# Kernel tuning notes

Measured on AMD Instinct MI355X. Metric: run time of the kernel, lower is better.

Reference implementation:

```python
import jax, jax.numpy as jnp
import numpy as np

EPS = 1e-20
K, STRIDE, PAD = 5, 2, 2
B, CIN, COUT, H, W = 4, 32, 32, 192, 192
HO = (H + 2 * PAD - K) // STRIDE + 1
WO = (W + 2 * PAD - K) // STRIDE + 1


def _patches(x, pad_value):
    # x: [B,C,H,W] -> [B,C,K*K,HO,WO]; same window layout as F.max_pool2d
    xp = jnp.pad(x, ((0, 0), (0, 0), (PAD, PAD), (PAD, PAD)), constant_values=pad_value)
    cols = [xp[:, :, dy:dy + STRIDE * HO:STRIDE, dx:dx + STRIDE * WO:STRIDE]
            for dy in range(K) for dx in range(K)]
    return jnp.stack(cols, axis=2)


def setup_inputs() -> dict:
    key = jax.random.key(0)
    ks = jax.random.split(key, 9)
    d = jax.random.uniform(ks[0], (B, CIN, H, W), jnp.float32, 0.05, 1.0)
    cd = jax.random.uniform(ks[1], (B, CIN, H, W), jnp.float32)
    s = jax.random.uniform(ks[2], (B, CIN, H, W), jnp.float32)
    cs = jax.random.uniform(ks[3], (B, CIN, H, W), jnp.float32)
    w_s_from_d = jax.random.normal(ks[4], (1, 1, 1, 1), jnp.float32) * 0.5
    w_prop = jax.random.normal(ks[5], (1, CIN, 1, 1), jnp.float32) * 0.5
    spatial_weight = jax.random.normal(ks[6], (CIN, 1, K, K), jnp.float32) * 0.5
    channel_weight = jax.random.normal(ks[7], (COUT, CIN, 1, 1), jnp.float32) * 0.5
    bias = jax.random.normal(ks[8], (1, COUT, 1, 1), jnp.float32) * 0.1
    return {"d": d, "cd": cd, "s": s, "cs": cs, "w_s_from_d": w_s_from_d,
            "w_prop": w_prop, "spatial_weight": spatial_weight,
            "channel_weight": channel_weight, "bias": bias}


def reference(d, cd, s, cs, w_s_from_d, w_prop, spatial_weight, channel_weight, bias):
    # EnforcePos reparameterization applied at forward time
    w_sfd = jax.nn.sigmoid(w_s_from_d)
    w_p = jax.nn.softplus(w_prop)
    sw = jax.nn.softplus(spatial_weight)   # [CIN,1,K,K] depthwise
    cw = jax.nn.softplus(channel_weight)   # [COUT,CIN,1,1]

    # max-pool argmax indices (torch pads with -inf), then gather d/cd at those indices
    j_max = jnp.argmax(_patches(d * cd, -jnp.inf), axis=2, keepdims=True)
    j_min = jnp.argmax(_patches(cd / (d + EPS), -jnp.inf), axis=2, keepdims=True)
    p_d = _patches(d, 0.0)
    p_cd = _patches(cd, 0.0)
    d_max = jnp.take_along_axis(p_d, j_max, axis=2)[:, :, 0]
    d_min = jnp.take_along_axis(p_d, j_min, axis=2)[:, :, 0]
    cd_max = jnp.take_along_axis(p_cd, j_max, axis=2)[:, :, 0]
    cd_min = jnp.take_along_axis(p_cd, j_min, axis=2)[:, :, 0]

    min_div_max = jnp.abs(d_min / (d_max + EPS))
    s_from_d = (1 - w_sfd) * min_div_max + w_sfd * min_div_max ** 2
    cs_from_d = cd_max * cd_min

    # stride > 1: no pre-propagation
    s_prop, cs_prop = s, cs

    dn = ('NCHW', 'OIHW', 'NCHW')
    def dwconv(x):  # depthwise 5x5, stride 2, pad 2
        return jax.lax.conv_general_dilated(
            x, sw, (STRIDE, STRIDE), [(PAD, PAD), (PAD, PAD)],
            feature_group_count=CIN, dimension_numbers=dn)

    nom = dwconv(cs_prop * s_prop)
    denom = dwconv(cs_prop)
    s_spatial = nom / (denom + EPS)
    cs_spatial = denom / (jnp.sum(sw) + EPS)

    cw2 = cw[:, :, 0, 0]  # [COUT,CIN], 1x1 conv == channel mixing
    nom = jnp.einsum('bihw,oi->bohw', cs_spatial * s_spatial, cw2)
    denom = jnp.einsum('bihw,oi->bohw', cs_spatial, cw2)
    s_out = nom / (denom + EPS)
    cs_out = denom / (jnp.sum(cw) + EPS)

    # stride > 1: merge pooled s_from_d afterwards
    s_out = (w_p * cs_out * s_out + cs_from_d * s_from_d) / (w_p * cs_out + cs_from_d + EPS)
    cs_out = (w_p * cs_out + cs_from_d) / (w_p + 1)

    s_out = s_out + bias
    s_out = jax.nn.sigmoid(s_out * 2 - 1) / 2 + 0.5
    return s_out, cs_out / (STRIDE * STRIDE)
```

## Files before the change

kernel.cpp:

```cpp
#include <hip/hip_runtime.h>

#define KK    5
#define PADV  2
#define NB    4
#define NC    32
#define NH    192
#define NW    192
#define NHO   96
#define NWO   96
#define NPX   (NHO * NWO)
#define NPLANE (NB * NC * NPX)
#define EPSF  1e-20f

__device__ __forceinline__ float softplusf(float x) {
    return fmaxf(x, 0.f) + log1pf(expf(-fabsf(x)));
}

#define TROWS 19
#define NJ    98
#define PLD4  100
#define K1T   768
#define ITEMS (TROWS * NJ)

__global__ __launch_bounds__(K1T, 6) void k1(
    const float* __restrict__ dg,
    const float* __restrict__ cdg,
    const float* __restrict__ sg,
    const float* __restrict__ csg,
    const float* __restrict__ wsfdg,
    const float* __restrict__ spwg,
    float4* __restrict__ ws4)
{
    __shared__ float4 st_e[TROWS][PLD4];
    __shared__ float4 st_o[TROWS][PLD4];
    __shared__ float sw_row[25];
    __shared__ float red[12];
    __shared__ float scal[2];

    const int t  = threadIdx.x;
    const int bx = blockIdx.x;
    const int c  = blockIdx.y;
    const int b  = blockIdx.z;

    const int gy0 = 16 * bx - 2;
    const size_t base = ((size_t)(b * NC) + c) * (NH * NW);

    float2 Ld[3], Lcd[3], Ls[3], Lcs[3];
    int   rr_[3], jj_[3];
    bool  okv[3], act[3];
#pragma unroll
    for (int k = 0; k < 3; k++) {
        const int it = t + k * K1T;
        act[k] = (it < ITEMS);
        const int r = act[k] ? (it / NJ) : 0;
        const int j = act[k] ? (it - r * NJ) : 0;
        rr_[k] = r; jj_[k] = j;
        const int gy = gy0 + r;
        const bool ok = act[k] && ((unsigned)gy < NH) && (j >= 1) && (j <= 96);
        okv[k] = ok;
        float2 z = make_float2(0.f, 0.f);
        Ld[k] = z; Lcd[k] = z; Ls[k] = z; Lcs[k] = z;
        if (ok) {
            const size_t idx = base + (size_t)gy * NW + (2 * j - 2);
            Ld[k]  = *(const float2*)(dg  + idx);
            Lcd[k] = *(const float2*)(cdg + idx);
            Ls[k]  = *(const float2*)(sg  + idx);
            Lcs[k] = *(const float2*)(csg + idx);
        }
    }

    float part = 0.f;
    for (int i = t; i < NC * 25; i += K1T) {
        float v = softplusf(spwg[i]);
        part += v;
        int cr = i - c * 25;
        if (cr >= 0 && cr < 25) sw_row[cr] = v;
    }
#pragma unroll
    for (int m = 32; m >= 1; m >>= 1) part += __shfl_xor(part, m, 64);
    if ((t & 63) == 0) red[t >> 6] = part;

#pragma unroll
    for (int k = 0; k < 3; k++) {
        if (act[k]) {
            float pme, pve, pmo, pvo;
            if (okv[k]) {
                pme = Ld[k].x * Lcd[k].x;
                pve = Lcd[k].x / (Ld[k].x + EPSF);
                pmo = Ld[k].y * Lcd[k].y;
                pvo = Lcd[k].y / (Ld[k].y + EPSF);
            } else {
                pme = -INFINITY; pve = -INFINITY; pmo = -INFINITY; pvo = -INFINITY;
            }
            const int r = rr_[k], j = jj_[k];
            st_e[r][j] = make_float4(pme, pve, Lcs[k].x, Lcs[k].x * Ls[k].x);
            st_o[r][j] = make_float4(pmo, pvo, Lcs[k].y, Lcs[k].y * Ls[k].y);
        }
    }
    __syncthreads();
    if (t == 0) {
        float acc = 0.f;
#pragma unroll
        for (int i = 0; i < 12; i++) acc += red[i];
        scal[0] = acc;
        scal[1] = 1.f / (1.f + expf(-wsfdg[0]));
    }
    __syncthreads();

    const int oyl = t / 96;
    const int ox  = t - oyl * 96;
    const int r0  = oyl * 2;

    float bm = -INFINITY, bv = -INFINITY;
    float pvm = 0.f, pmn = 0.f;
    float nom = 0.f, den = 0.f;

#pragma unroll
    for (int dy = 0; dy < 5; dy++) {
        const int r = r0 + dy;
        const float w0 = sw_row[dy * 5 + 0];
        const float w1 = sw_row[dy * 5 + 1];
        const float w2 = sw_row[dy * 5 + 2];
        const float w3 = sw_row[dy * 5 + 3];
        const float w4 = sw_row[dy * 5 + 4];

        const float4 E0 = st_e[r][ox];
        const float4 O0 = st_o[r][ox];
        const float4 E1 = st_e[r][ox + 1];
        const float4 O1 = st_o[r][ox + 1];
        const float4 E2 = st_e[r][ox + 2];

        if (E0.x > bm) { bm = E0.x; pvm = E0.y; }
        if (E0.y > bv) { bv = E0.y; pmn = E0.x; }
        if (O0.x > bm) { bm = O0.x; pvm = O0.y; }
        if (O0.y > bv) { bv = O0.y; pmn = O0.x; }
        if (E1.x > bm) { bm = E1.x; pvm = E1.y; }
        if (E1.y > bv) { bv = E1.y; pmn = E1.x; }
        if (O1.x > bm) { bm = O1.x; pvm = O1.y; }
        if (O1.y > bv) { bv = O1.y; pmn = O1.x; }
        if (E2.x > bm) { bm = E2.x; pvm = E2.y; }
        if (E2.y > bv) { bv = E2.y; pmn = E2.x; }

        nom += w0 * E0.w; den += w0 * E0.z;
        nom += w1 * O0.w; den += w1 * O0.z;
        nom += w2 * E1.w; den += w2 * E1.z;
        nom += w3 * O1.w; den += w3 * O1.z;
        nom += w4 * E2.w; den += w4 * E2.z;
    }

    const float t1 = pmn * pvm;
    const float t2 = bv * bm;
    const float mdm = fabsf(sqrtf(t1 / t2));
    const float cfd = sqrtf(t1 * t2);

    const float sumsw = scal[0];
    const float wsfd  = scal[1];
    const float sfd  = (1.f - wsfd) * mdm + wsfd * mdm * mdm;
    const float ssp  = nom / (den + EPSF);
    const float cssp = den / (sumsw + EPSF);

    const int opx = (8 * bx + oyl) * NWO + ox;
    const size_t oidx = ((size_t)(b * NC) + c) * NPX + opx;
    ws4[oidx] = make_float4(cssp * ssp, cssp, sfd, cfd);
}

#define K2PX 32

__global__ __launch_bounds__(256, 8) void k2(
    const float4* __restrict__ ws4,
    const float* __restrict__ wpropg,
    const float* __restrict__ chwg,
    const float* __restrict__ biasg,
    float* __restrict__ out)
{
    __shared__ float cw_s[NC * NC];
    __shared__ float wp_s[NC];
    __shared__ float bias_s[NC];
    __shared__ float A_s[NC][K2PX + 1];
    __shared__ float B_s[NC][K2PX + 1];
    __shared__ float S_s[NC][K2PX + 1];
    __shared__ float C_s[NC][K2PX + 1];
    __shared__ float red[4];
    __shared__ float scal[1];

    const int t    = threadIdx.x;
    const int b    = blockIdx.y;
    const int px0  = blockIdx.x * K2PX;
    const int p    = t & (K2PX - 1);
    const int slot = t >> 5;

    float part = 0.f;
    for (int i = t; i < NC * NC; i += 256) {
        float v = softplusf(chwg[i]); cw_s[i] = v; part += v;
    }
    if (t < NC) { wp_s[t] = softplusf(wpropg[t]); bias_s[t] = biasg[t]; }
#pragma unroll
    for (int m = 32; m >= 1; m >>= 1) part += __shfl_xor(part, m, 64);
    if ((t & 63) == 0) red[t >> 6] = part;

    const size_t bb = (size_t)b * NC * NPX;
#pragma unroll
    for (int idx = 0; idx < NC * K2PX; idx += 256) {
        const int i  = (idx + t) >> 5;
        const int pp = (idx + t) & (K2PX - 1);
        const float4 q = ws4[bb + (size_t)i * NPX + px0 + pp];
        A_s[i][pp] = q.x;
        B_s[i][pp] = q.y;
        S_s[i][pp] = q.z;
        C_s[i][pp] = q.w;
    }
    __syncthreads();
    if (t == 0) scal[0] = red[0] + red[1] + red[2] + red[3];
    __syncthreads();

    const float sumcw = scal[0];
    const int px = px0 + p;

    float nom2[4], den2[4];
#pragma unroll
    for (int k = 0; k < 4; k++) { nom2[k] = 0.f; den2[k] = 0.f; }

#pragma unroll
    for (int i = 0; i < NC; i++) {
        const float a  = A_s[i][p];
        const float b2 = B_s[i][p];
#pragma unroll
        for (int k = 0; k < 4; k++) {
            const float w = cw_s[(slot + 8 * k) * NC + i];
            nom2[k] += w * a;
            den2[k] += w * b2;
        }
    }

#pragma unroll
    for (int k = 0; k < 4; k++) {
        const int o = slot + 8 * k;
        const float sfd = S_s[o][p];
        const float cfd = C_s[o][p];

        const float smix  = nom2[k] / (den2[k] + EPSF);
        const float csmix = den2[k] / (sumcw + EPSF);
        const float wp    = wp_s[o];

        float sout = (wp * csmix * smix + cfd * sfd) / (wp * csmix + cfd + EPSF);
        const float csout = (wp * csmix + cfd) / (wp + 1.f);

        sout += bias_s[o];
        sout = 1.f / (1.f + expf(-(sout * 2.f - 1.f))) * 0.5f + 0.5f;

        const size_t oidx = bb + (size_t)o * NPX + px;
        out[oidx]                  = sout;
        out[(size_t)NPLANE + oidx] = csout * 0.25f;
    }
}

#define TW    8
#define TH    4
#define TPP   33

__global__ __launch_bounds__(256, 4) void fused_kernel(
    const float* __restrict__ dg,
    const float* __restrict__ cdg,
    const float* __restrict__ sg,
    const float* __restrict__ csg,
    const float* __restrict__ wsfdg,
    const float* __restrict__ wpropg,
    const float* __restrict__ spwg,
    const float* __restrict__ chwg,
    const float* __restrict__ biasg,
    float* __restrict__ out)
{
    __shared__ float sw_s[NC * 25];
    __shared__ float cw_s[NC * NC];
    __shared__ float wp_s[NC];
    __shared__ float bias_s[NC];
    __shared__ float A_s[NC][TPP];
    __shared__ float B_s[NC][TPP];
    __shared__ float S_s[NC][TPP];
    __shared__ float C_s[NC][TPP];
    __shared__ float red[8];
    __shared__ float scal[3];

    const int t = threadIdx.x;
    const int b = blockIdx.z;
    const int tile_x = blockIdx.x * TW;
    const int tile_y = blockIdx.y * TH;

    float p_sw = 0.f, p_cw = 0.f;
    for (int i = t; i < NC * 25; i += 256) { float v = softplusf(spwg[i]); sw_s[i] = v; p_sw += v; }
    for (int i = t; i < NC * NC; i += 256) { float v = softplusf(chwg[i]); cw_s[i] = v; p_cw += v; }
    if (t < NC) { wp_s[t] = softplusf(wpropg[t]); bias_s[t] = biasg[t]; }
#pragma unroll
    for (int m = 32; m >= 1; m >>= 1) {
        p_sw += __shfl_xor(p_sw, m, 64);
        p_cw += __shfl_xor(p_cw, m, 64);
    }
    if ((t & 63) == 0) { red[(t >> 6) * 2] = p_sw; red[(t >> 6) * 2 + 1] = p_cw; }
    __syncthreads();
    if (t == 0) {
        scal[0] = red[0] + red[2] + red[4] + red[6];
        scal[1] = red[1] + red[3] + red[5] + red[7];
        scal[2] = 1.f / (1.f + expf(-wsfdg[0]));
    }
    __syncthreads();

    const float sumsw = scal[0];
    const float sumcw = scal[1];
    const float wsfd  = scal[2];

    const int c  = t >> 3;
    const int tr = (t >> 2) & 1;
    const int q  = t & 3;
    const int oy0 = tile_y + tr * 2;
    const int ox0 = tile_x + q * 2;
    const int cb = ox0 * 2 - 2;
    const int rb = oy0 * 2 - 2;
    const size_t base = ((size_t)(b * NC) + c) * NH * NW;
    const float* __restrict__ dp  = dg  + base;
    const float* __restrict__ cdp = cdg + base;
    const float* __restrict__ sp  = sg  + base;
    const float* __restrict__ csp = csg + base;

    bool slotok[4];
#pragma unroll
    for (int k = 0; k < 4; k++) slotok[k] = (cb + 2 * k >= 0) && (cb + 2 * k + 1 < NW);
    bool ciok[7];
#pragma unroll
    for (int ci = 0; ci < 7; ci++) ciok[ci] = ((unsigned)(cb + ci) < NW);

    float bm[2][2], dM[2][2], cM[2][2];
    float bn[2][2], dN[2][2], cN[2][2];
    float nom[2][2], den[2][2];
#pragma unroll
    for (int r = 0; r < 2; r++)
#pragma unroll
        for (int q2 = 0; q2 < 2; q2++) {
            bm[r][q2] = -INFINITY; bn[r][q2] = -INFINITY;
            dM[r][q2] = 0.f; cM[r][q2] = 0.f; dN[r][q2] = 0.f; cN[r][q2] = 0.f;
            nom[r][q2] = 0.f; den[r][q2] = 0.f;
        }

#pragma unroll
    for (int rr = 0; rr < 7; rr++) {
        const int iy = rb + rr;
        if ((unsigned)iy < NH) {
            const int roff = iy * NW + cb;
            float dv[8], cdv[8], sv[8], csv[8];
#pragma unroll
            for (int k = 0; k < 4; k++) {
                float2 vD, vCD, vS, vCS;
                if (slotok[k]) {
                    vD  = *(const float2*)(dp  + roff + 2 * k);
                    vCD = *(const float2*)(cdp + roff + 2 * k);
                    vS  = *(const float2*)(sp  + roff + 2 * k);
                    vCS = *(const float2*)(csp + roff + 2 * k);
                } else {
                    vD = make_float2(0.f, 0.f); vCD = vD; vS = vD; vCS = vD;
                }
                dv[2*k] = vD.x;  dv[2*k+1] = vD.y;
                cdv[2*k] = vCD.x; cdv[2*k+1] = vCD.y;
                sv[2*k] = vS.x;  sv[2*k+1] = vS.y;
                csv[2*k] = vCS.x; csv[2*k+1] = vCS.y;
            }
            float pm[7], pv[7];
#pragma unroll
            for (int ci = 0; ci < 7; ci++) {
                pm[ci] = dv[ci] * cdv[ci];
                pv[ci] = cdv[ci] / (dv[ci] + EPSF);
            }
#pragma unroll
            for (int r = 0; r < 2; r++) {
                const int dy = rr - 2 * r;
                if (dy >= 0 && dy <= 4) {
#pragma unroll
                    for (int dx = 0; dx < 5; dx++) {
                        const float w = sw_s[c * 25 + dy * 5 + dx];
#pragma unroll
                        for (int q2 = 0; q2 < 2; q2++) {
                            const int ci = 2 * q2 + dx;
                            if (ciok[ci]) {
                                if (pm[ci] > bm[r][q2]) { bm[r][q2] = pm[ci]; dM[r][q2] = dv[ci]; cM[r][q2] = cdv[ci]; }
                                if (pv[ci] > bn[r][q2]) { bn[r][q2] = pv[ci]; dN[r][q2] = dv[ci]; cN[r][q2] = cdv[ci]; }
                                nom[r][q2] += w * (csv[ci] * sv[ci]);
                                den[r][q2] += w * csv[ci];
                            }
                        }
                    }
                }
            }
        }
    }

#pragma unroll
    for (int r = 0; r < 2; r++)
#pragma unroll
        for (int q2 = 0; q2 < 2; q2++) {
            const float mdm  = fabsf(dN[r][q2] / (dM[r][q2] + EPSF));
            const float sfd  = (1.f - wsfd) * mdm + wsfd * mdm * mdm;
            const float cfd  = cM[r][q2] * cN[r][q2];
            const float ssp  = nom[r][q2] / (den[r][q2] + EPSF);
            const float cssp = den[r][q2] / (sumsw + EPSF);
            const int p = (tr * 2 + r) * TW + (q * 2 + q2);
            A_s[c][p] = cssp * ssp;
            B_s[c][p] = cssp;
            S_s[c][p] = sfd;
            C_s[c][p] = cfd;
        }
    __syncthreads();

    const int p  = t & 31;
    const int o0 = t >> 5;
    const int py = p >> 3;
    const int pxx = p & 7;
    const int opx = (tile_y + py) * NWO + tile_x + pxx;

    float nom2[4], den2[4];
#pragma unroll
    for (int k = 0; k < 4; k++) { nom2[k] = 0.f; den2[k] = 0.f; }

#pragma unroll
    for (int i = 0; i < NC; i++) {
        const float a  = A_s[i][p];
        const float b2 = B_s[i][p];
#pragma unroll
        for (int k = 0; k < 4; k++) {
            const float w = cw_s[(o0 + 8 * k) * NC + i];
            nom2[k] += w * a;
            den2[k] += w * b2;
        }
    }

#pragma unroll
    for (int k = 0; k < 4; k++) {
        const int o = o0 + 8 * k;
        const float smix  = nom2[k] / (den2[k] + EPSF);
        const float csmix = den2[k] / (sumcw + EPSF);
        const float wp    = wp_s[o];
        const float sfd   = S_s[o][p];
        const float cfd   = C_s[o][p];

        float sout = (wp * csmix * smix + cfd * sfd) / (wp * csmix + cfd + EPSF);
        const float csout = (wp * csmix + cfd) / (wp + 1.f);

        sout += bias_s[o];
        sout = 1.f / (1.f + expf(-(sout * 2.f - 1.f))) * 0.5f + 0.5f;

        const int oidx = ((b * NC) + o) * NPX + opx;
        out[oidx]          = sout;
        out[NPLANE + oidx] = csout * 0.25f;
    }
}

extern "C" void kernel_launch(void* const* d_in, const int* in_sizes, int n_in,
                              void* d_out, int out_size, void* d_ws, size_t ws_size,
                              hipStream_t stream) {
    const float* d     = (const float*)d_in[0];
    const float* cd    = (const float*)d_in[1];
    const float* s     = (const float*)d_in[2];
    const float* cs    = (const float*)d_in[3];
    const float* wsfd  = (const float*)d_in[4];
    const float* wprop = (const float*)d_in[5];
    const float* spw   = (const float*)d_in[6];
    const float* chw   = (const float*)d_in[7];
    const float* bias  = (const float*)d_in[8];
    float* out = (float*)d_out;

    const size_t need = (size_t)4 * NPLANE * sizeof(float);
    if (ws_size >= need) {
        float4* ws4 = (float4*)d_ws;
        k1<<<dim3(NHO / 8, NC, NB), K1T, 0, stream>>>(d, cd, s, cs, wsfd, spw, ws4);
        k2<<<dim3(NPX / K2PX, NB), 256, 0, stream>>>(ws4, wprop, chw, bias, out);
    } else {
        fused_kernel<<<dim3(NWO / TW, NHO / TH, NB), 256, 0, stream>>>(
            d, cd, s, cs, wsfd, wprop, spw, chw, bias, out);
    }
}
```

Baseline: 41.45 us.

## Process three row strips per k1 block with register-prefetched next strip

Each k1 block now handles three consecutive 8-output-row strips instead of one, cutting the grid from 12 to 4 blocks along the row dimension. The global loads for the next strip are issued into registers while the current strip's pooling and depthwise conv run from shared memory, overlapping memory latency with compute. The per-block softplus weight setup and reduction is amortized over three strips. In exchange the grid has a third as many blocks (512), which may reduce occupancy and latency hiding across the GPU, and an extra barrier is added per strip.

```diff
diff --git a/kernel.cpp b/kernel.cpp
--- a/kernel.cpp
+++ b/kernel.cpp
@@ -20,6 +20,7 @@
 #define NJ    98
 #define PLD4  100
 #define K1T   768
+#define SPB   3
 #define ITEMS (TROWS * NJ)
 
 __global__ __launch_bounds__(K1T, 6) void k1(
@@ -38,16 +39,13 @@
     __shared__ float scal[2];
 
     const int t  = threadIdx.x;
-    const int bx = blockIdx.x;
+    const int sg0 = blockIdx.x * SPB;
     const int c  = blockIdx.y;
     const int b  = blockIdx.z;
-
-    const int gy0 = 16 * bx - 2;
     const size_t base = ((size_t)(b * NC) + c) * (NH * NW);
 
-    float2 Ld[3], Lcd[3], Ls[3], Lcs[3];
-    int   rr_[3], jj_[3];
-    bool  okv[3], act[3];
+    int  rr_[3], jj_[3];
+    bool act[3], jok[3];
 #pragma unroll
     for (int k = 0; k < 3; k++) {
         const int it = t + k * K1T;
@@ -55,17 +53,27 @@
         const int r = act[k] ? (it / NJ) : 0;
         const int j = act[k] ? (it - r * NJ) : 0;
         rr_[k] = r; jj_[k] = j;
-        const int gy = gy0 + r;
-        const bool ok = act[k] && ((unsigned)gy < NH) && (j >= 1) && (j <= 96);
-        okv[k] = ok;
-        float2 z = make_float2(0.f, 0.f);
-        Ld[k] = z; Lcd[k] = z; Ls[k] = z; Lcs[k] = z;
-        if (ok) {
-            const size_t idx = base + (size_t)gy * NW + (2 * j - 2);
-            Ld[k]  = *(const float2*)(dg  + idx);
-            Lcd[k] = *(const float2*)(cdg + idx);
-            Ls[k]  = *(const float2*)(sg  + idx);
-            Lcs[k] = *(const float2*)(csg + idx);
+        jok[k] = (j >= 1) && (j <= 96);
+    }
+
+    float2 Ld[3], Lcd[3], Ls[3], Lcs[3];
+    bool okv[3];
+    {
+        const int gy0 = 16 * sg0 - 2;
+#pragma unroll
+        for (int k = 0; k < 3; k++) {
+            const int gy = gy0 + rr_[k];
+            const bool ok = act[k] && ((unsigned)gy < NH) && jok[k];
+            okv[k] = ok;
+            float2 z = make_float2(0.f, 0.f);
+            Ld[k] = z; Lcd[k] = z; Ls[k] = z; Lcs[k] = z;
+            if (ok) {
+                const size_t idx = base + (size_t)gy * NW + (2 * jj_[k] - 2);
+                Ld[k]  = *(const float2*)(dg  + idx);
+                Lcd[k] = *(const float2*)(cdg + idx);
+                Ls[k]  = *(const float2*)(sg  + idx);
+                Lcs[k] = *(const float2*)(csg + idx);
+            }
         }
     }
 
@@ -79,24 +87,6 @@
 #pragma unroll
     for (int m = 32; m >= 1; m >>= 1) part += __shfl_xor(part, m, 64);
     if ((t & 63) == 0) red[t >> 6] = part;
-
-#pragma unroll
-    for (int k = 0; k < 3; k++) {
-        if (act[k]) {
-            float pme, pve, pmo, pvo;
-            if (okv[k]) {
-                pme = Ld[k].x * Lcd[k].x;
-                pve = Lcd[k].x / (Ld[k].x + EPSF);
-                pmo = Ld[k].y * Lcd[k].y;
-                pvo = Lcd[k].y / (Ld[k].y + EPSF);
-            } else {
-                pme = -INFINITY; pve = -INFINITY; pmo = -INFINITY; pvo = -INFINITY;
-            }
-            const int r = rr_[k], j = jj_[k];
-            st_e[r][j] = make_float4(pme, pve, Lcs[k].x, Lcs[k].x * Ls[k].x);
-            st_o[r][j] = make_float4(pmo, pvo, Lcs[k].y, Lcs[k].y * Ls[k].y);
-        }
-    }
     __syncthreads();
     if (t == 0) {
         float acc = 0.f;
@@ -106,62 +96,106 @@
         scal[1] = 1.f / (1.f + expf(-wsfdg[0]));
     }
     __syncthreads();
+    const float sumsw = scal[0];
+    const float wsfd  = scal[1];
 
     const int oyl = t / 96;
     const int ox  = t - oyl * 96;
     const int r0  = oyl * 2;
 
-    float bm = -INFINITY, bv = -INFINITY;
-    float pvm = 0.f, pmn = 0.f;
-    float nom = 0.f, den = 0.f;
-
-#pragma unroll
-    for (int dy = 0; dy < 5; dy++) {
-        const int r = r0 + dy;
-        const float w0 = sw_row[dy * 5 + 0];
-        const float w1 = sw_row[dy * 5 + 1];
-        const float w2 = sw_row[dy * 5 + 2];
-        const float w3 = sw_row[dy * 5 + 3];
-        const float w4 = sw_row[dy * 5 + 4];
-
-        const float4 E0 = st_e[r][ox];
-        const float4 O0 = st_o[r][ox];
-        const float4 E1 = st_e[r][ox + 1];
-        const float4 O1 = st_o[r][ox + 1];
-        const float4 E2 = st_e[r][ox + 2];
-
-        if (E0.x > bm) { bm = E0.x; pvm = E0.y; }
-        if (E0.y > bv) { bv = E0.y; pmn = E0.x; }
-        if (O0.x > bm) { bm = O0.x; pvm = O0.y; }
-        if (O0.y > bv) { bv = O0.y; pmn = O0.x; }
-        if (E1.x > bm) { bm = E1.x; pvm = E1.y; }
-        if (E1.y > bv) { bv = E1.y; pmn = E1.x; }
-        if (O1.x > bm) { bm = O1.x; pvm = O1.y; }
-        if (O1.y > bv) { bv = O1.y; pmn = O1.x; }
-        if (E2.x > bm) { bm = E2.x; pvm = E2.y; }
-        if (E2.y > bv) { bv = E2.y; pmn = E2.x; }
-
-        nom += w0 * E0.w; den += w0 * E0.z;
-        nom += w1 * O0.w; den += w1 * O0.z;
-        nom += w2 * E1.w; den += w2 * E1.z;
-        nom += w3 * O1.w; den += w3 * O1.z;
-        nom += w4 * E2.w; den += w4 * E2.z;
-    }
-
-    const float t1 = pmn * pvm;
-    const float t2 = bv * bm;
-    const float mdm = fabsf(sqrtf(t1 / t2));
-    const float cfd = sqrtf(t1 * t2);
-
-    const float sumsw = scal[0];
-    const float wsfd  = scal[1];
-    const float sfd  = (1.f - wsfd) * mdm + wsfd * mdm * mdm;
-    const float ssp  = nom / (den + EPSF);
-    const float cssp = den / (sumsw + EPSF);
-
-    const int opx = (8 * bx + oyl) * NWO + ox;
-    const size_t oidx = ((size_t)(b * NC) + c) * NPX + opx;
-    ws4[oidx] = make_float4(cssp * ssp, cssp, sfd, cfd);
+    for (int sidx = 0; sidx < SPB; sidx++) {
+        const int strip = sg0 + sidx;
+
+        if (sidx > 0) __syncthreads();
+
+#pragma unroll
+        for (int k = 0; k < 3; k++) {
+            if (act[k]) {
+                float pme, pve, pmo, pvo;
+                if (okv[k]) {
+                    pme = Ld[k].x * Lcd[k].x;
+                    pve = Lcd[k].x / (Ld[k].x + EPSF);
+                    pmo = Ld[k].y * Lcd[k].y;
+                    pvo = Lcd[k].y / (Ld[k].y + EPSF);
+                } else {
+                    pme = -INFINITY; pve = -INFINITY; pmo = -INFINITY; pvo = -INFINITY;
+                }
+                const int r = rr_[k], j = jj_[k];
+                st_e[r][j] = make_float4(pme, pve, Lcs[k].x, Lcs[k].x * Ls[k].x);
+                st_o[r][j] = make_float4(pmo, pvo, Lcs[k].y, Lcs[k].y * Ls[k].y);
+            }
+        }
+        __syncthreads();
+
+        if (sidx + 1 < SPB) {
+            const int gy0n = 16 * (strip + 1) - 2;
+#pragma unroll
+            for (int k = 0; k < 3; k++) {
+                const int gy = gy0n + rr_[k];
+                const bool ok = act[k] && ((unsigned)gy < NH) && jok[k];
+                okv[k] = ok;
+                float2 z = make_float2(0.f, 0.f);
+                Ld[k] = z; Lcd[k] = z; Ls[k] = z; Lcs[k] = z;
+                if (ok) {
+                    const size_t idx = base + (size_t)gy * NW + (2 * jj_[k] - 2);
+                    Ld[k]  = *(const float2*)(dg  + idx);
+                    Lcd[k] = *(const float2*)(cdg + idx);
+                    Ls[k]  = *(const float2*)(sg  + idx);
+                    Lcs[k] = *(const float2*)(csg + idx);
+                }
+            }
+        }
+
+        float bm = -INFINITY, bv = -INFINITY;
+        float pvm = 0.f, pmn = 0.f;
+        float nom = 0.f, den = 0.f;
+
+#pragma unroll
+        for (int dy = 0; dy < 5; dy++) {
+            const int r = r0 + dy;
+            const float w0 = sw_row[dy * 5 + 0];
+            const float w1 = sw_row[dy * 5 + 1];
+            const float w2 = sw_row[dy * 5 + 2];
+            const float w3 = sw_row[dy * 5 + 3];
+            const float w4 = sw_row[dy * 5 + 4];
+
+            const float4 E0 = st_e[r][ox];
+            const float4 O0 = st_o[r][ox];
+            const float4 E1 = st_e[r][ox + 1];
+            const float4 O1 = st_o[r][ox + 1];
+            const float4 E2 = st_e[r][ox + 2];
+
+            if (E0.x > bm) { bm = E0.x; pvm = E0.y; }
+            if (E0.y > bv) { bv = E0.y; pmn = E0.x; }
+            if (O0.x > bm) { bm = O0.x; pvm = O0.y; }
+            if (O0.y > bv) { bv = O0.y; pmn = O0.x; }
+            if (E1.x > bm) { bm = E1.x; pvm = E1.y; }
+            if (E1.y > bv) { bv = E1.y; pmn = E1.x; }
+            if (O1.x > bm) { bm = O1.x; pvm = O1.y; }
+            if (O1.y > bv) { bv = O1.y; pmn = O1.x; }
+            if (E2.x > bm) { bm = E2.x; pvm = E2.y; }
+            if (E2.y > bv) { bv = E2.y; pmn = E2.x; }
+
+            nom += w0 * E0.w; den += w0 * E0.z;
+            nom += w1 * O0.w; den += w1 * O0.z;
+            nom += w2 * E1.w; den += w2 * E1.z;
+            nom += w3 * O1.w; den += w3 * O1.z;
+            nom += w4 * E2.w; den += w4 * E2.z;
+        }
+
+        const float t1 = pmn * pvm;
+        const float t2 = bv * bm;
+        const float mdm = fabsf(sqrtf(t1 / t2));
+        const float cfd = sqrtf(t1 * t2);
+
+        const float sfd  = (1.f - wsfd) * mdm + wsfd * mdm * mdm;
+        const float ssp  = nom / (den + EPSF);
+        const float cssp = den / (sumsw + EPSF);
+
+        const int opx = (8 * strip + oyl) * NWO + ox;
+        const size_t oidx = ((size_t)(b * NC) + c) * NPX + opx;
+        ws4[oidx] = make_float4(cssp * ssp, cssp, sfd, cfd);
+    }
 }
 
 #define K2PX 32
@@ -468,7 +502,7 @@
     const size_t need = (size_t)4 * NPLANE * sizeof(float);
     if (ws_size >= need) {
         float4* ws4 = (float4*)d_ws;
-        k1<<<dim3(NHO / 8, NC, NB), K1T, 0, stream>>>(d, cd, s, cs, wsfd, spw, ws4);
+        k1<<<dim3(4, NC, NB), K1T, 0, stream>>>(d, cd, s, cs, wsfd, spw, ws4);
         k2<<<dim3(NPX / K2PX, NB), 256, 0, stream>>>(ws4, wprop, chw, bias, out);
     } else {
         fused_kernel<<<dim3(NWO / TW, NHO / TH, NB), 256, 0, stream>>>(
```

New measurement: 42.91 us. 3.5% more time.
